# Optimization experiments

Hardware: AMD Instinct MI355X
Metric: run time of the kernel (lower is better)

## Reference

```python
import jax, jax.numpy as jnp
import numpy as np

B, N, C_IN, T = 16, 1024, 2, 12
HID, K_CHEB, KT = 64, 3, 3
OUT, PRED = 32, 12
E = 16384
BN_EPS = 1e-5


def _conv(x, w, b):
    # x: (B,C,N,T), w: (O,I,1,kt) -> (B,O,N,T-kt+1)
    y = jax.lax.conv_general_dilated(x, w, (1, 1), 'VALID',
                                     dimension_numbers=('NCHW', 'OIHW', 'NCHW'))
    return y + b[None, :, None, None]


def temporal_conv(X, w1, b1, w2, b2, w3, b3):
    # X: (B,T,N,C) -> (B,T',N,O) with gated GLU-style conv
    x = jnp.transpose(X, (0, 3, 2, 1))  # (B,C,N,T)
    P = _conv(x, w1, b1)
    Q = jax.nn.sigmoid(_conv(x, w2, b2))
    H = jax.nn.relu(P * Q + _conv(x, w3, b3))
    return jnp.transpose(H, (0, 3, 2, 1))


def cheb_conv(x, edge_index, edge_weight, W, b, num_nodes):
    # x: (B,T,N,H); ChebConv with sym normalization, lambda_max=2 => L_hat = -D^-1/2 A D^-1/2
    row, col = edge_index[0], edge_index[1]
    w = jnp.where(row == col, 0.0, edge_weight)  # remove self loops
    deg = jax.ops.segment_sum(w, row, num_segments=num_nodes)
    dinv = jnp.where(deg > 0, jax.lax.rsqrt(jnp.where(deg > 0, deg, 1.0)), 0.0)
    norm = -(dinv[row] * w * dinv[col])  # (E,)

    def prop(z):  # z: (B,T,N,H) -> L_hat @ z along node axis
        return jnp.zeros_like(z).at[:, :, col, :].add(z[:, :, row, :] * norm[:, None])

    Tx0 = x
    out = jnp.einsum('btnh,hf->btnf', Tx0, W[0])
    Tx1 = prop(x)
    out = out + jnp.einsum('btnh,hf->btnf', Tx1, W[1])
    for k in range(2, W.shape[0]):
        Tx2 = 2.0 * prop(Tx1) - Tx0
        out = out + jnp.einsum('btnh,hf->btnf', Tx2, W[k])
        Tx0, Tx1 = Tx1, Tx2
    return out + b


def setup_inputs() -> dict:
    key = jax.random.key(0)
    ks = jax.random.split(key, 20)
    s = 0.1
    inp = {
        'X': jax.random.normal(ks[0], (B, N, C_IN, T), dtype=jnp.float32),
        'edge_index': jax.random.randint(ks[1], (2, E), 0, N),
        'edge_weight': jax.random.uniform(ks[2], (E,), dtype=jnp.float32),
        # temporal conv 1: C_IN -> HID
        'tc1_w1': s * jax.random.normal(ks[3], (HID, C_IN, 1, KT)),
        'tc1_b1': jnp.zeros((HID,)),
        'tc1_w2': s * jax.random.normal(ks[4], (HID, C_IN, 1, KT)),
        'tc1_b2': jnp.zeros((HID,)),
        'tc1_w3': s * jax.random.normal(ks[5], (HID, C_IN, 1, KT)),
        'tc1_b3': jnp.zeros((HID,)),
        # cheb conv
        'cheb_W': s * jax.random.normal(ks[6], (K_CHEB, HID, HID)),
        'cheb_b': jnp.zeros((HID,)),
        # temporal conv 2: HID -> OUT*PRED
        'tc2_w1': s * jax.random.normal(ks[7], (OUT * PRED, HID, 1, KT)),
        'tc2_b1': jnp.zeros((OUT * PRED,)),
        'tc2_w2': s * jax.random.normal(ks[8], (OUT * PRED, HID, 1, KT)),
        'tc2_b2': jnp.zeros((OUT * PRED,)),
        'tc2_w3': s * jax.random.normal(ks[9], (OUT * PRED, HID, 1, KT)),
        'tc2_b3': jnp.zeros((OUT * PRED,)),
        # batch norm over node channel
        'bn_gamma': jnp.ones((N,)),
        'bn_beta': jnp.zeros((N,)),
    }
    return inp


def reference(X, edge_index, edge_weight,
              tc1_w1, tc1_b1, tc1_w2, tc1_b2, tc1_w3, tc1_b3,
              cheb_W, cheb_b,
              tc2_w1, tc2_b1, tc2_w2, tc2_b2, tc2_w3, tc2_b3,
              bn_gamma, bn_beta):
    Xp = jnp.transpose(X, (0, 3, 1, 2))  # (B,T,N,C_in)
    batch, seq_len, num_nodes, _ = Xp.shape
    T0 = temporal_conv(Xp, tc1_w1, tc1_b1, tc1_w2, tc1_b2, tc1_w3, tc1_b3)  # (B,T-2,N,HID)
    Tg = jax.nn.relu(cheb_conv(T0, edge_index, edge_weight, cheb_W, cheb_b, num_nodes))
    T2 = temporal_conv(Tg, tc2_w1, tc2_b1, tc2_w2, tc2_b2, tc2_w3, tc2_b3)  # (B,T-4,N,OUT*PRED)
    T3 = jnp.transpose(T2, (0, 2, 1, 3))  # (B,N,T'',Cout); BN channel = node
    mean = jnp.mean(T3, axis=(0, 2, 3), keepdims=True)
    var = jnp.var(T3, axis=(0, 2, 3), keepdims=True)
    bn = (T3 - mean) * jax.lax.rsqrt(var + BN_EPS)
    bn = bn * bn_gamma[None, :, None, None] + bn_beta[None, :, None, None]
    T4 = jnp.transpose(bn, (3, 0, 1, 2))[..., -1]  # (Cout,B,N)
    return T4.reshape(seq_len, batch, num_nodes, -1)  # (T,B,N,OUT)
```

## Files before the change

### kernel.cpp

```cpp
#include <hip/hip_runtime.h>


typedef __bf16 bf16;
typedef __bf16 bf16x8 __attribute__((ext_vector_type(8)));
typedef float  f32x4  __attribute__((ext_vector_type(4)));

__device__ __forceinline__ f32x4 mfma16(bf16x8 a, bf16x8 b, f32x4 c) {
  return __builtin_amdgcn_mfma_f32_16x16x32_bf16(a, b, c, 0, 0, 0);
}
__device__ __forceinline__ f32x4 splat4(float v) { f32x4 t = {v, v, v, v}; return t; }

__device__ __forceinline__ void lds_load16(const bf16* g, bf16* l) {
  __builtin_amdgcn_global_load_lds((const __attribute__((address_space(1))) void*)g,
                                   (__attribute__((address_space(3))) void*)l, 16, 0, 0);
}

#define NN 1024
#define EE 16384

__global__ __launch_bounds__(256) void deg_kernel(const int* __restrict__ ei,
                                                  const float* __restrict__ ew,
                                                  float* __restrict__ deg) {
  int e = blockIdx.x * 256 + threadIdx.x;
  int r = ei[e], c = ei[EE + e];
  if (r != c) atomicAdd(&deg[r], ew[e]);
}

__global__ __launch_bounds__(256) void scatterL_kernel(const int* __restrict__ ei,
                                                       const float* __restrict__ ew,
                                                       const float* __restrict__ deg,
                                                       float* __restrict__ Lf) {
  int e = blockIdx.x * 256 + threadIdx.x;
  int r = ei[e], c = ei[EE + e];
  float w = (r == c) ? 0.0f : ew[e];
  float dr = deg[r], dc = deg[c];
  float ir = dr > 0.0f ? rsqrtf(dr) : 0.0f;
  float ic = dc > 0.0f ? rsqrtf(dc) : 0.0f;
  float norm = -(ir * w * ic);
  if (norm != 0.0f) atomicAdd(&Lf[(size_t)c * NN + r], norm);
}

__global__ __launch_bounds__(256) void cvtL_kernel(const float* __restrict__ Lf,
                                                   bf16* __restrict__ Lbf) {
  int i = blockIdx.x * 256 + threadIdx.x;
  Lbf[i] = (bf16)Lf[i];
}

__global__ __launch_bounds__(256) void wprep_kernel(const float* __restrict__ W,
                                                    const float* __restrict__ w21,
                                                    const float* __restrict__ w22,
                                                    const float* __restrict__ w23,
                                                    float* __restrict__ Wc,
                                                    bf16* __restrict__ W2c) {
  int i = blockIdx.x * 256 + threadIdx.x;
  if (i < 12288) {
    int row = i >> 6, j = i & 63;
    int src = row >> 6, h = row & 63;
    float v;
    if (src == 0)      v = W[h * 64 + j] - W[2 * 4096 + h * 64 + j];
    else if (src == 1) v = W[4096 + h * 64 + j];
    else               v = 2.0f * W[2 * 4096 + h * 64 + j];
    Wc[i] = v;
  } else {
    int j2 = i - 12288;
    int c = j2 / 192, k = j2 % 192;
    int og = c / 48, r48 = c % 48;
    int conv = r48 >> 4, oo = r48 & 15;
    int o = og * 16 + oo;
    int kk = k >> 6, h = k & 63;
    const float* ws = (conv == 0) ? w21 : (conv == 1) ? w22 : w23;
    W2c[j2] = (bf16)ws[(o * 64 + h) * 3 + kk];
  }
}

__global__ __launch_bounds__(256) void tc1_kernel(const float* __restrict__ X,
                                                  const float* __restrict__ w1, const float* __restrict__ c1,
                                                  const float* __restrict__ w2, const float* __restrict__ c2,
                                                  const float* __restrict__ w3, const float* __restrict__ c3,
                                                  bf16* __restrict__ zf) {
  int row = blockIdx.y;
  int n = blockIdx.x * 256 + threadIdx.x;
  int h = row & 63, bt = row >> 6;
  int t = bt % 10, b = bt / 10;
  float P = c1[h], Q = c2[h], R = c3[h];
  const float* xb = X + (size_t)(b * 1024 + n) * 24;
  #pragma unroll
  for (int c = 0; c < 2; c++)
    #pragma unroll
    for (int k = 0; k < 3; k++) {
      float xv = xb[c * 12 + t + k];
      int wi = (h * 2 + c) * 3 + k;
      P += xv * w1[wi]; Q += xv * w2[wi]; R += xv * w3[wi];
    }
  float Hv = P * (1.0f / (1.0f + __expf(-Q))) + R;
  Hv = Hv > 0.0f ? Hv : 0.0f;
  zf[(size_t)row * NN + n] = (bf16)Hv;
}

__global__ __launch_bounds__(256) void gemm_bt(const bf16* __restrict__ A,
                                               const bf16* __restrict__ Bt,
                                               bf16* __restrict__ C,
                                               int M, int Nc, int K) {
  __shared__ __align__(16) bf16 As[8192];
  __shared__ __align__(16) bf16 Bs[8192];
  const int tid = threadIdx.x, lane = tid & 63, w = tid >> 6;
  const int wm = w >> 1, wn = w & 1;
  const int m0 = blockIdx.y * 128, n0 = blockIdx.x * 128;
  const int colL = lane & 15, kg = lane >> 4;
  const int rxor = colL & 7;

  f32x4 acc[4][4];
  #pragma unroll
  for (int i = 0; i < 4; i++)
    #pragma unroll
    for (int j = 0; j < 4; j++) acc[i][j] = splat4(0.0f);

  for (int kb = 0; kb < K; kb += 64) {
    if (kb) __syncthreads();
    #pragma unroll
    for (int i = 0; i < 4; i++) {
      int e = (w * 4 + i) * 512 + lane * 8;
      int row = e >> 6, s = (e >> 3) & 7;
      int ksw = ((s ^ (row & 7)) << 3);
      lds_load16(&A[(size_t)(m0 + row) * K + kb + ksw], &As[(w * 4 + i) * 512]);
      lds_load16(&Bt[(size_t)(n0 + row) * K + kb + ksw], &Bs[(w * 4 + i) * 512]);
    }
    __syncthreads();
    #pragma unroll
    for (int kk = 0; kk < 2; kk++) {
      bf16x8 af[4], bfr[4];
      #pragma unroll
      for (int mt = 0; mt < 4; mt++)
        af[mt] = *(const bf16x8*)(&As[(wm * 64 + mt * 16 + colL) * 64 +
                                      (((kk * 4 + kg) ^ rxor) << 3)]);
      #pragma unroll
      for (int nt = 0; nt < 4; nt++)
        bfr[nt] = *(const bf16x8*)(&Bs[(wn * 64 + nt * 16 + colL) * 64 +
                                       (((kk * 4 + kg) ^ rxor) << 3)]);
      #pragma unroll
      for (int mt = 0; mt < 4; mt++)
        #pragma unroll
        for (int nt = 0; nt < 4; nt++)
          acc[mt][nt] = mfma16(af[mt], bfr[nt], acc[mt][nt]);
    }
  }
  #pragma unroll
  for (int mt = 0; mt < 4; mt++)
    #pragma unroll
    for (int nt = 0; nt < 4; nt++) {
      int m = m0 + wm * 64 + mt * 16 + kg * 4;
      int n = n0 + wn * 64 + nt * 16 + colL;
      #pragma unroll
      for (int r = 0; r < 4; r++)
        C[(size_t)(m + r) * Nc + n] = (bf16)acc[mt][nt][r];
    }
}

__global__ __launch_bounds__(256) void combine_kernel(const bf16* __restrict__ zf,
                                                      const bf16* __restrict__ P1f,
                                                      const bf16* __restrict__ P2f,
                                                      const float* __restrict__ Wc,
                                                      const float* __restrict__ chebb,
                                                      bf16* __restrict__ Tg) {
  const int slab = blockIdx.y;
  const int b = slab / 10, t = slab % 10;
  const int lane = threadIdx.x & 63;
  const int jg = __builtin_amdgcn_readfirstlane(threadIdx.x >> 6);
  const int n = blockIdx.x * 64 + lane;

  float acc[16];
  #pragma unroll
  for (int j = 0; j < 16; j++) acc[j] = chebb[jg * 16 + j];

  const size_t zoff = (size_t)(slab * 64) * NN + n;
  #pragma unroll 1
  for (int src = 0; src < 3; src++) {
    const bf16* Z = (src == 0) ? zf : (src == 1) ? P1f : P2f;
    const float* wsrc = Wc + (size_t)(src * 64) * 64 + jg * 16;
    #pragma unroll 4
    for (int h = 0; h < 64; h++) {
      float v = (float)Z[zoff + (size_t)h * NN];
      const float* wr = wsrc + h * 64;
      #pragma unroll
      for (int j = 0; j < 16; j++) acc[j] += v * wr[j];
    }
  }

  bf16 tmp[16];
  #pragma unroll
  for (int j = 0; j < 16; j++) {
    float x = acc[j];
    tmp[j] = (bf16)(x > 0.0f ? x : 0.0f);
  }
  size_t base = (size_t)((n * 16 + b) * 10 + t) * 64 + jg * 16;
  *(bf16x8*)(&Tg[base])     = *(const bf16x8*)(&tmp[0]);
  *(bf16x8*)(&Tg[base + 8]) = *(const bf16x8*)(&tmp[8]);
}

__global__ __launch_bounds__(256) void tc2_kernel(const bf16* __restrict__ Tg,
                                                  const bf16* __restrict__ W2c,
                                                  const float* __restrict__ b1,
                                                  const float* __restrict__ b2,
                                                  const float* __restrict__ b3,
                                                  float* __restrict__ nsum,
                                                  float* __restrict__ nsq,
                                                  bf16* __restrict__ slice) {
  __shared__ __align__(16) char smem[40960];
  bf16* As = (bf16*)smem;
  bf16* Ws = (bf16*)(smem + 16384);
  const int rb = blockIdx.x, cho = blockIdx.y;
  const int b = rb >> 6, tpp = (rb >> 3) & 7, n0 = (rb & 7) << 7;
  const int tid = threadIdx.x, lane = tid & 63, w = tid >> 6;
  const int wm = w >> 1, wn = w & 1;
  const int colL = lane & 15, kg = lane >> 4;
  const int rxor = colL & 7;

  f32x4 acc[4][6];
  #pragma unroll
  for (int i = 0; i < 4; i++)
    #pragma unroll
    for (int j = 0; j < 6; j++) acc[i][j] = splat4(0.0f);

  for (int kb = 0; kb < 192; kb += 64) {
    if (kb) __syncthreads();
    #pragma unroll
    for (int i = 0; i < 4; i++) {
      int e = (w * 4 + i) * 512 + lane * 8;
      int row = e >> 6, s = (e >> 3) & 7;
      int ksw = ((s ^ (row & 7)) << 3);
      lds_load16(&Tg[(size_t)((n0 + row) * 16 + b) * 640 + tpp * 64 + kb + ksw],
                 &As[(w * 4 + i) * 512]);
    }
    #pragma unroll
    for (int i = 0; i < 6; i++) {
      int e = (w * 6 + i) * 512 + lane * 8;
      int col = e >> 6, s = (e >> 3) & 7;
      int ksw = ((s ^ (col & 7)) << 3);
      lds_load16(&W2c[(size_t)(cho * 192 + col) * 192 + kb + ksw],
                 &Ws[(w * 6 + i) * 512]);
    }
    __syncthreads();
    #pragma unroll
    for (int kk = 0; kk < 2; kk++) {
      bf16x8 af[4], bfr[6];
      #pragma unroll
      for (int mt = 0; mt < 4; mt++)
        af[mt] = *(const bf16x8*)(&As[(wm * 64 + mt * 16 + colL) * 64 +
                                      (((kk * 4 + kg) ^ rxor) << 3)]);
      #pragma unroll
      for (int j = 0; j < 6; j++)
        bfr[j] = *(const bf16x8*)(&Ws[(wn * 96 + j * 16 + colL) * 64 +
                                      (((kk * 4 + kg) ^ rxor) << 3)]);
      #pragma unroll
      for (int mt = 0; mt < 4; mt++)
        #pragma unroll
        for (int j = 0; j < 6; j++)
          acc[mt][j] = mfma16(af[mt], bfr[j], acc[mt][j]);
    }
  }

  float ssum[4][4], ssq[4][4];
  #pragma unroll
  for (int mt = 0; mt < 4; mt++)
    #pragma unroll
    for (int r = 0; r < 4; r++) { ssum[mt][r] = 0.0f; ssq[mt][r] = 0.0f; }

  float bv1[2], bv2[2], bv3[2];
  int obase[2];
  #pragma unroll
  for (int g = 0; g < 2; g++) {
    int o = ((cho * 4 + wn * 2 + g) << 4) + colL;
    obase[g] = o;
    bv1[g] = b1[o]; bv2[g] = b2[o]; bv3[g] = b3[o];
  }

  #pragma unroll
  for (int mt = 0; mt < 4; mt++)
    #pragma unroll
    for (int g = 0; g < 2; g++) {
      int o = obase[g];
      #pragma unroll
      for (int r = 0; r < 4; r++) {
        float p  = acc[mt][g * 3 + 0][r] + bv1[g];
        float q  = acc[mt][g * 3 + 1][r] + bv2[g];
        float rr = acc[mt][g * 3 + 2][r] + bv3[g];
        float h = p * (1.0f / (1.0f + __expf(-q))) + rr;
        h = h > 0.0f ? h : 0.0f;
        ssum[mt][r] += h;
        ssq[mt][r] += h * h;
        if (tpp == 7) {
          int n = n0 + wm * 64 + mt * 16 + kg * 4 + r;
          slice[(size_t)((b << 10) + n) * 384 + o] = (bf16)h;
        }
      }
    }

  __syncthreads();
  float* sred = (float*)smem;
  if (tid < 256) { sred[tid] = 0.0f; }
  __syncthreads();
  #pragma unroll
  for (int mt = 0; mt < 4; mt++)
    #pragma unroll
    for (int r = 0; r < 4; r++) {
      float s = ssum[mt][r], q = ssq[mt][r];
      #pragma unroll
      for (int d = 1; d < 16; d <<= 1) {
        s += __shfl_xor(s, d);
        q += __shfl_xor(q, d);
      }
      if (colL == 0) {
        int rl = wm * 64 + mt * 16 + kg * 4 + r;
        atomicAdd(&sred[rl * 2], s);
        atomicAdd(&sred[rl * 2 + 1], q);
      }
    }
  __syncthreads();
  if (tid < 128) {
    atomicAdd(&nsum[n0 + tid], sred[tid * 2]);
    atomicAdd(&nsq[n0 + tid], sred[tid * 2 + 1]);
  }
}

__global__ __launch_bounds__(256) void bnstat_kernel(const float* __restrict__ nsum,
                                                     const float* __restrict__ nsq,
                                                     const float* __restrict__ gamma,
                                                     const float* __restrict__ beta,
                                                     float* __restrict__ scoff) {
  int n = blockIdx.x * 256 + threadIdx.x;
  const float inv_cnt = 1.0f / 49152.0f;
  float m = nsum[n] * inv_cnt;
  float var = nsq[n] * inv_cnt - m * m;
  float sc = rsqrtf(var + 1e-5f) * gamma[n];
  scoff[n] = sc;
  scoff[1024 + n] = beta[n] - m * sc;
}

__global__ __launch_bounds__(256) void final_kernel(const bf16* __restrict__ slice,
                                                    const float* __restrict__ scoff,
                                                    float* __restrict__ out) {
  int f = blockIdx.x * 256 + threadIdx.x;
  int c = f >> 14, rem = f & 16383;
  int b = rem >> 10, n = rem & 1023;
  out[f] = (float)slice[(size_t)((b << 10) + n) * 384 + c] * scoff[n] + scoff[1024 + n];
}

extern "C" void kernel_launch(void* const* d_in, const int* in_sizes, int n_in,
                              void* d_out, int out_size, void* d_ws, size_t ws_size,
                              hipStream_t stream) {
  const float* X    = (const float*)d_in[0];
  const int*   ei   = (const int*)d_in[1];
  const float* ew   = (const float*)d_in[2];
  const float* t1w1 = (const float*)d_in[3];
  const float* t1b1 = (const float*)d_in[4];
  const float* t1w2 = (const float*)d_in[5];
  const float* t1b2 = (const float*)d_in[6];
  const float* t1w3 = (const float*)d_in[7];
  const float* t1b3 = (const float*)d_in[8];
  const float* chebW = (const float*)d_in[9];
  const float* chebB = (const float*)d_in[10];
  const float* t2w1 = (const float*)d_in[11];
  const float* t2b1 = (const float*)d_in[12];
  const float* t2w2 = (const float*)d_in[13];
  const float* t2b2 = (const float*)d_in[14];
  const float* t2w3 = (const float*)d_in[15];
  const float* t2b3 = (const float*)d_in[16];
  const float* gamma = (const float*)d_in[17];
  const float* beta  = (const float*)d_in[18];
  float* out = (float*)d_out;

  char* ws = (char*)d_ws;
  float* Lf    = (float*)(ws);
  float* deg   = (float*)(ws + 4194304);
  float* nsum  = (float*)(ws + 4198400);
  float* nsq   = (float*)(ws + 4202496);
  bf16*  Lbf   = (bf16*)(ws + 4210688);
  bf16*  zf    = (bf16*)(ws + 6307840);
  bf16*  P1f   = (bf16*)(ws + 27279360);
  bf16*  P2f   = (bf16*)(ws + 48250880);
  bf16*  Tg    = (bf16*)(ws + 69222400);
  float* Wc    = (float*)(ws + 90193920);
  bf16*  W2c   = (bf16*)(ws + 90243072);
  bf16*  slice = (bf16*)(ws + 90685440);
  float* scoff = (float*)(ws + 103268352);

  hipMemsetAsync(ws, 0, 4206592, stream);

  wprep_kernel<<<912, 256, 0, stream>>>(chebW, t2w1, t2w2, t2w3, Wc, W2c);
  tc1_kernel<<<dim3(4, 10240), 256, 0, stream>>>(X, t1w1, t1b1, t1w2, t1b2, t1w3, t1b3, zf);
  deg_kernel<<<64, 256, 0, stream>>>(ei, ew, deg);
  scatterL_kernel<<<64, 256, 0, stream>>>(ei, ew, deg, Lf);
  cvtL_kernel<<<4096, 256, 0, stream>>>(Lf, Lbf);
  gemm_bt<<<dim3(8, 80), 256, 0, stream>>>(zf, Lbf, P1f, 10240, 1024, 1024);
  gemm_bt<<<dim3(8, 80), 256, 0, stream>>>(P1f, Lbf, P2f, 10240, 1024, 1024);
  combine_kernel<<<dim3(16, 160), 256, 0, stream>>>(zf, P1f, P2f, Wc, chebB, Tg);
  tc2_kernel<<<dim3(1024, 6), 256, 0, stream>>>(Tg, W2c, t2b1, t2b2, t2b3, nsum, nsq, slice);
  bnstat_kernel<<<4, 256, 0, stream>>>(nsum, nsq, gamma, beta, scoff);
  final_kernel<<<24576, 256, 0, stream>>>(slice, scoff, out);
}
```

Baseline: 391.5 us.

## Restructure tc2 to keep A tile resident and loop over all output chunks

```diff
diff --git a/kernel.cpp b/kernel.cpp
--- a/kernel.cpp
+++ b/kernel.cpp
@@ -197,7 +197,7 @@
   *(bf16x8*)(&Tg[base + 8]) = *(const bf16x8*)(&tmp[8]);
 }
 
-__global__ __launch_bounds__(256) void tc2_kernel(const bf16* __restrict__ Tg,
+__global__ __launch_bounds__(512) void tc2_kernel(const bf16* __restrict__ Tg,
                                                   const bf16* __restrict__ W2c,
                                                   const float* __restrict__ b1,
                                                   const float* __restrict__ b2,
@@ -205,99 +205,101 @@
                                                   float* __restrict__ nsum,
                                                   float* __restrict__ nsq,
                                                   bf16* __restrict__ slice) {
-  __shared__ __align__(16) char smem[40960];
-  bf16* As = (bf16*)smem;
-  bf16* Ws = (bf16*)(smem + 16384);
-  const int rb = blockIdx.x, cho = blockIdx.y;
-  const int b = rb >> 6, tpp = (rb >> 3) & 7, n0 = (rb & 7) << 7;
+  __shared__ __align__(16) char smem[147456];
+  bf16* Asm = (bf16*)smem;
+  const int rb = blockIdx.x;
+  const int b = rb >> 5, tpp = (rb >> 2) & 7, n0 = (rb & 3) << 8;
   const int tid = threadIdx.x, lane = tid & 63, w = tid >> 6;
   const int wm = w >> 1, wn = w & 1;
   const int colL = lane & 15, kg = lane >> 4;
   const int rxor = colL & 7;
 
-  f32x4 acc[4][6];
-  #pragma unroll
-  for (int i = 0; i < 4; i++)
-    #pragma unroll
-    for (int j = 0; j < 6; j++) acc[i][j] = splat4(0.0f);
-
-  for (int kb = 0; kb < 192; kb += 64) {
-    if (kb) __syncthreads();
-    #pragma unroll
-    for (int i = 0; i < 4; i++) {
-      int e = (w * 4 + i) * 512 + lane * 8;
-      int row = e >> 6, s = (e >> 3) & 7;
-      int ksw = ((s ^ (row & 7)) << 3);
-      lds_load16(&Tg[(size_t)((n0 + row) * 16 + b) * 640 + tpp * 64 + kb + ksw],
-                 &As[(w * 4 + i) * 512]);
-    }
-    #pragma unroll
-    for (int i = 0; i < 6; i++) {
-      int e = (w * 6 + i) * 512 + lane * 8;
-      int col = e >> 6, s = (e >> 3) & 7;
-      int ksw = ((s ^ (col & 7)) << 3);
-      lds_load16(&W2c[(size_t)(cho * 192 + col) * 192 + kb + ksw],
-                 &Ws[(w * 6 + i) * 512]);
-    }
-    __syncthreads();
-    #pragma unroll
-    for (int kk = 0; kk < 2; kk++) {
-      bf16x8 af[4], bfr[6];
-      #pragma unroll
-      for (int mt = 0; mt < 4; mt++)
-        af[mt] = *(const bf16x8*)(&As[(wm * 64 + mt * 16 + colL) * 64 +
-                                      (((kk * 4 + kg) ^ rxor) << 3)]);
-      #pragma unroll
-      for (int j = 0; j < 6; j++)
-        bfr[j] = *(const bf16x8*)(&Ws[(wn * 96 + j * 16 + colL) * 64 +
-                                      (((kk * 4 + kg) ^ rxor) << 3)]);
+  #pragma unroll
+  for (int i = 0; i < 12; i++) {
+    int fb = w * 12288 + i * 1024 + lane * 16;
+    int row = fb / 384;
+    int s = (fb % 384) >> 4;
+    int koff = (s & ~7) * 8 + (((s & 7) ^ (row & 7)) << 3);
+    lds_load16(&Tg[(size_t)((n0 + row) * 16 + b) * 640 + tpp * 64 + koff],
+               (bf16*)(smem + w * 12288 + i * 1024));
+  }
+  auto stageW = [&](int cho, int ks, int buf) {
+    #pragma unroll
+    for (int i = 0; i < 3; i++) {
+      int fb = w * 3072 + i * 1024 + lane * 16;
+      int col = fb >> 7;
+      int s8 = (fb >> 4) & 7;
+      lds_load16(&W2c[(size_t)(cho * 192 + col) * 192 + ks * 64 + ((s8 ^ (col & 7)) << 3)],
+                 (bf16*)(smem + 98304 + buf * 24576 + w * 3072 + i * 1024));
+    }
+  };
+  stageW(0, 0, 0);
+  __syncthreads();
+
+  float ssum[4][4], ssq[4][4];
+  #pragma unroll
+  for (int mt = 0; mt < 4; mt++)
+    #pragma unroll
+    for (int r = 0; r < 4; r++) { ssum[mt][r] = 0.0f; ssq[mt][r] = 0.0f; }
+
+  #pragma unroll
+  for (int cho = 0; cho < 6; cho++) {
+    f32x4 acc[4][6];
+    #pragma unroll
+    for (int i = 0; i < 4; i++)
+      #pragma unroll
+      for (int j = 0; j < 6; j++) acc[i][j] = splat4(0.0f);
+
+    #pragma unroll
+    for (int ks = 0; ks < 3; ks++) {
+      const int p = cho * 3 + ks;
+      if (p < 17) stageW((p + 1) / 3, (p + 1) % 3, (p + 1) & 1);
+      const bf16* Wsb = (const bf16*)(smem + 98304 + (p & 1) * 24576);
+      #pragma unroll
+      for (int kk = 0; kk < 2; kk++) {
+        bf16x8 af[4], bfr[6];
+        #pragma unroll
+        for (int mt = 0; mt < 4; mt++)
+          af[mt] = *(const bf16x8*)(&Asm[(wm * 64 + mt * 16 + colL) * 192 + ks * 64 +
+                                         (((kk * 4 + kg) ^ rxor) << 3)]);
+        #pragma unroll
+        for (int j = 0; j < 6; j++)
+          bfr[j] = *(const bf16x8*)(&Wsb[(wn * 96 + j * 16 + colL) * 64 +
+                                         (((kk * 4 + kg) ^ rxor) << 3)]);
+        #pragma unroll
+        for (int mt = 0; mt < 4; mt++)
+          #pragma unroll
+          for (int j = 0; j < 6; j++)
+            acc[mt][j] = mfma16(af[mt], bfr[j], acc[mt][j]);
+      }
+      __syncthreads();
+    }
+
+    #pragma unroll
+    for (int g = 0; g < 2; g++) {
+      int o = ((cho * 4 + wn * 2 + g) << 4) + colL;
+      float bv1 = b1[o], bv2 = b2[o], bv3 = b3[o];
       #pragma unroll
       for (int mt = 0; mt < 4; mt++)
         #pragma unroll
-        for (int j = 0; j < 6; j++)
-          acc[mt][j] = mfma16(af[mt], bfr[j], acc[mt][j]);
-    }
-  }
-
-  float ssum[4][4], ssq[4][4];
-  #pragma unroll
-  for (int mt = 0; mt < 4; mt++)
-    #pragma unroll
-    for (int r = 0; r < 4; r++) { ssum[mt][r] = 0.0f; ssq[mt][r] = 0.0f; }
-
-  float bv1[2], bv2[2], bv3[2];
-  int obase[2];
-  #pragma unroll
-  for (int g = 0; g < 2; g++) {
-    int o = ((cho * 4 + wn * 2 + g) << 4) + colL;
-    obase[g] = o;
-    bv1[g] = b1[o]; bv2[g] = b2[o]; bv3[g] = b3[o];
-  }
-
-  #pragma unroll
-  for (int mt = 0; mt < 4; mt++)
-    #pragma unroll
-    for (int g = 0; g < 2; g++) {
-      int o = obase[g];
-      #pragma unroll
-      for (int r = 0; r < 4; r++) {
-        float p  = acc[mt][g * 3 + 0][r] + bv1[g];
-        float q  = acc[mt][g * 3 + 1][r] + bv2[g];
-        float rr = acc[mt][g * 3 + 2][r] + bv3[g];
-        float h = p * (1.0f / (1.0f + __expf(-q))) + rr;
-        h = h > 0.0f ? h : 0.0f;
-        ssum[mt][r] += h;
-        ssq[mt][r] += h * h;
-        if (tpp == 7) {
-          int n = n0 + wm * 64 + mt * 16 + kg * 4 + r;
-          slice[(size_t)((b << 10) + n) * 384 + o] = (bf16)h;
+        for (int r = 0; r < 4; r++) {
+          float p  = acc[mt][g * 3 + 0][r] + bv1;
+          float q  = acc[mt][g * 3 + 1][r] + bv2;
+          float rr = acc[mt][g * 3 + 2][r] + bv3;
+          float h = p * (1.0f / (1.0f + __expf(-q))) + rr;
+          h = h > 0.0f ? h : 0.0f;
+          ssum[mt][r] += h;
+          ssq[mt][r] += h * h;
+          if (tpp == 7) {
+            int n = n0 + wm * 64 + mt * 16 + kg * 4 + r;
+            slice[(size_t)((b << 10) + n) * 384 + o] = (bf16)h;
+          }
         }
-      }
-    }
-
-  __syncthreads();
+    }
+  }
+
   float* sred = (float*)smem;
-  if (tid < 256) { sred[tid] = 0.0f; }
+  sred[tid] = 0.0f;
   __syncthreads();
   #pragma unroll
   for (int mt = 0; mt < 4; mt++)
@@ -316,7 +318,7 @@
       }
     }
   __syncthreads();
-  if (tid < 128) {
+  if (tid < 256) {
     atomicAdd(&nsum[n0 + tid], sred[tid * 2]);
     atomicAdd(&nsq[n0 + tid], sred[tid * 2 + 1]);
   }
@@ -394,7 +396,7 @@
   gemm_bt<<<dim3(8, 80), 256, 0, stream>>>(zf, Lbf, P1f, 10240, 1024, 1024);
   gemm_bt<<<dim3(8, 80), 256, 0, stream>>>(P1f, Lbf, P2f, 10240, 1024, 1024);
   combine_kernel<<<dim3(16, 160), 256, 0, stream>>>(zf, P1f, P2f, Wc, chebB, Tg);
-  tc2_kernel<<<dim3(1024, 6), 256, 0, stream>>>(Tg, W2c, t2b1, t2b2, t2b3, nsum, nsq, slice);
+  tc2_kernel<<<512, 512, 0, stream>>>(Tg, W2c, t2b1, t2b2, t2b3, nsum, nsq, slice);
   bnstat_kernel<<<4, 256, 0, stream>>>(nsum, nsq, gamma, beta, scoff);
   final_kernel<<<24576, 256, 0, stream>>>(slice, scoff, out);
 }
```

Result: slower. 488.6 us (+24.8%).
